# Optimization experiments

Measured on AMD Instinct MI355X. Metric: run time of the kernel, lower is better.

Reference implementation:

```python
import jax, jax.numpy as jnp
import numpy as np
import math

DIM = 1024
N_HEADS = 16
HEAD_DIM = DIM // N_HEADS  # 64
BATCH = 16
SEQ = 512


def _rope_tables(seq_len, head_dim, dtype=jnp.float32):
    inv_freq = 1.0 / (10000.0 ** (jnp.arange(0, head_dim, 2, dtype=jnp.float32) / head_dim))
    t = jnp.arange(seq_len, dtype=jnp.float32)
    freqs = jnp.outer(t, inv_freq)            # [S, head_dim/2]
    emb = jnp.concatenate([freqs, freqs], -1)  # [S, head_dim]
    return jnp.cos(emb).astype(dtype), jnp.sin(emb).astype(dtype)


def _rotate_half(x):
    x1, x2 = x[..., : x.shape[-1] // 2], x[..., x.shape[-1] // 2 :]
    return jnp.concatenate([-x2, x1], axis=-1)


def setup_inputs() -> dict:
    key = jax.random.key(0)
    ks = jax.random.split(key, 5)
    scale = 1.0 / math.sqrt(DIM)
    return {
        "x": jax.random.normal(ks[0], (BATCH, SEQ, DIM), dtype=jnp.float32),
        "Wq": jax.random.normal(ks[1], (DIM, DIM), dtype=jnp.float32) * scale,
        "Wk": jax.random.normal(ks[2], (DIM, DIM), dtype=jnp.float32) * scale,
        "Wv": jax.random.normal(ks[3], (DIM, DIM), dtype=jnp.float32) * scale,
        "Wo": jax.random.normal(ks[4], (DIM, DIM), dtype=jnp.float32) * scale,
    }


def reference(x, Wq, Wk, Wv, Wo):
    B, S, D = x.shape
    H, Hd = N_HEADS, HEAD_DIM
    # projections (nn.Linear: x @ W.T), then [B, H, S, Hd]
    q = (x @ Wq.T).reshape(B, S, H, Hd).transpose(0, 2, 1, 3)
    k = (x @ Wk.T).reshape(B, S, H, Hd).transpose(0, 2, 1, 3)
    v = (x @ Wv.T).reshape(B, S, H, Hd).transpose(0, 2, 1, 3)

    cos, sin = _rope_tables(S, Hd, x.dtype)  # [S, Hd], broadcasts over B, H
    q = q * cos + _rotate_half(q) * sin
    k = k * cos + _rotate_half(k) * sin

    scores = jnp.einsum("bhqd,bhkd->bhqk", q, k) / math.sqrt(Hd)
    causal = jnp.tril(jnp.ones((S, S), dtype=bool))
    scores = jnp.where(causal, scores, -jnp.inf)
    attn = jax.nn.softmax(scores, axis=-1)
    out = jnp.einsum("bhqk,bhkd->bhqd", attn, v)
    out = out.transpose(0, 2, 1, 3).reshape(B, S, D)
    return out @ Wo.T
```

## Files before the change

### kernel.cpp

```cpp
#include <hip/hip_runtime.h>

#define DIM 1024
#define NH 16
#define HD 64
#define BATCH 16
#define SEQ 512
#define MROWS (BATCH*SEQ)

using u16 = unsigned short;
using u32 = unsigned int;
typedef __attribute__((ext_vector_type(8))) u16 u16x8;
typedef __attribute__((ext_vector_type(4))) u16 u16x4;
typedef __attribute__((ext_vector_type(8))) __bf16 bf16x8;
typedef __attribute__((ext_vector_type(4))) float f32x4;
typedef __attribute__((ext_vector_type(4))) float float4v;

__device__ __forceinline__ float bf2f(u16 h) {
  unsigned u = ((unsigned)h) << 16;
  union { unsigned u; float f; } v; v.u = u; return v.f;
}
__device__ __forceinline__ u16 f2bf(float f) {
  union { float f; unsigned u; } v; v.f = f;
  unsigned u = v.u + 0x7fffu + ((v.u >> 16) & 1u);
  return (u16)(u >> 16);
}
__device__ __forceinline__ int swz(int r) { return (r & 7) ^ (r >> 3); }

__device__ __forceinline__ void gld_lds16(const u16* g, u16* l) {
  __builtin_amdgcn_global_load_lds(
      (const __attribute__((address_space(1))) void*)g,
      (__attribute__((address_space(3))) void*)l, 16, 0, 0);
}

__device__ __forceinline__ f32x4 mfma16(u16x8 a, u16x8 b, f32x4 c) {
  return __builtin_amdgcn_mfma_f32_16x16x32_bf16(
      __builtin_bit_cast(bf16x8, a), __builtin_bit_cast(bf16x8, b), c, 0, 0, 0);
}

__global__ void f32_to_bf16_kernel(const float* __restrict__ in, u16* __restrict__ out, int n) {
  int i = (blockIdx.x * blockDim.x + threadIdx.x) * 4;
  if (i >= n) return;
  float4v v = *(const float4v*)(in + i);
  u16x4 o;
  o.x = f2bf(v.x); o.y = f2bf(v.y); o.z = f2bf(v.z); o.w = f2bf(v.w);
  *(u16x4*)(out + i) = o;
}

__global__ void wconv_kernel(const float* __restrict__ Wq, const float* __restrict__ Wk,
                             const float* __restrict__ Wv, const float* __restrict__ Wo,
                             u16* __restrict__ out) {
  const float* in = (blockIdx.z == 0) ? Wq : (blockIdx.z == 1) ? Wk
                   : (blockIdx.z == 2) ? Wv : Wo;
  int i = (blockIdx.x * blockDim.x + threadIdx.x) * 4;
  float4v v = *(const float4v*)(in + i);
  u16x4 o;
  o.x = f2bf(v.x); o.y = f2bf(v.y); o.z = f2bf(v.z); o.w = f2bf(v.w);
  *(u16x4*)(out + (size_t)blockIdx.z * (DIM * DIM) + i) = o;
}

__global__ void rope_tables_kernel(float* __restrict__ ctab, float* __restrict__ stab) {
  int t = blockIdx.x * blockDim.x + threadIdx.x;
  int s = t >> 5, j = t & 31;
  float invf = powf(10000.f, -(float)j / 32.f);
  float a = (float)s * invf;
  ctab[t] = cosf(a);
  stab[t] = sinf(a);
}

__global__ void rope_kernel(u16* __restrict__ Q, u16* __restrict__ K,
                            const float* __restrict__ ctab, const float* __restrict__ stab) {
  int t = blockIdx.x * blockDim.x + threadIdx.x;
  u16* X = blockIdx.z ? K : Q;
  int j = t & 3;
  int h = (t >> 2) & 15;
  int m = t >> 6;
  int s = m & (SEQ - 1);
  u16* base = X + (size_t)m * DIM + h * HD + j * 8;
  u16x8 lo = *(u16x8*)base;
  u16x8 hi = *(u16x8*)(base + 32);
  const float* cp = ctab + s * 32 + j * 8;
  const float* sp = stab + s * 32 + j * 8;
  u16x8 lo2, hi2;
#pragma unroll
  for (int i = 0; i < 8; i++) {
    float c = cp[i], sn = sp[i];
    float xl = bf2f(lo[i]), xh = bf2f(hi[i]);
    lo2[i] = f2bf(xl * c - xh * sn);
    hi2[i] = f2bf(xh * c + xl * sn);
  }
  *(u16x8*)base = lo2;
  *(u16x8*)(base + 32) = hi2;
}

#define BM 128
#define BN 128

__global__ __launch_bounds__(256, 4) void gemm_qkv(const u16* __restrict__ A,
                                                   const u16* __restrict__ Bw,
                                                   u16* __restrict__ Cq, u16* __restrict__ Ck,
                                                   u16* __restrict__ Cv) {
  __shared__ alignas(16) u16 As[BM * 64];
  __shared__ alignas(16) u16 Bs[BN * 64];
  const int K = DIM, N = DIM;
  const int orig = blockIdx.x;
  const int id2 = (orig & 7) * 192 + (orig >> 3);
  const int m0 = (id2 / 24) * BM;
  const int n0g = (id2 % 24) * BN;
  u16* C = (n0g < 1024) ? Cq : (n0g < 2048) ? Ck : Cv;
  const int n0 = n0g & 1023;
  const int tid = threadIdx.x, lane = tid & 63;
  const int w = tid >> 6, wr = w >> 1, wc = w & 1;
  const int lr = lane & 15, kgrp = lane >> 4;

  f32x4 acc[4][4] = {};

  for (int kt = 0; kt < K; kt += 64) {
#pragma unroll
    for (int i = 0; i < 4; i++) {
      int c = tid + i * 256;
      int r_ = c >> 3, p = c & 7;
      gld_lds16(A + (size_t)(m0 + r_) * K + kt + ((p ^ (r_ & 7)) << 3), &As[c * 8]);
    }
#pragma unroll
    for (int i = 0; i < 4; i++) {
      int c = tid + i * 256;
      int r_ = c >> 3, p = c & 7;
      gld_lds16(Bw + (size_t)(n0g + r_) * K + kt + ((p ^ (r_ & 7)) << 3), &Bs[c * 8]);
    }
    __syncthreads();
#pragma unroll
    for (int half = 0; half < 2; half++) {
      u16x8 a[4], b[4];
      int g = half * 4 + kgrp;
#pragma unroll
      for (int i = 0; i < 4; i++) {
        int row = wr * 64 + i * 16 + lr;
        a[i] = *(const u16x8*)(&As[row * 64 + ((g ^ (row & 7)) << 3)]);
      }
#pragma unroll
      for (int j = 0; j < 4; j++) {
        int row = wc * 64 + j * 16 + lr;
        b[j] = *(const u16x8*)(&Bs[row * 64 + ((g ^ (row & 7)) << 3)]);
      }
#pragma unroll
      for (int i = 0; i < 4; i++)
#pragma unroll
        for (int j = 0; j < 4; j++)
          acc[i][j] = mfma16(a[i], b[j], acc[i][j]);
    }
    __syncthreads();
  }

#pragma unroll
  for (int i = 0; i < 4; i++) {
    int grow = m0 + wr * 64 + i * 16 + kgrp * 4;
#pragma unroll
    for (int j = 0; j < 4; j++) {
      int gcol = n0 + wc * 64 + j * 16 + lr;
#pragma unroll
      for (int r = 0; r < 4; r++)
        C[(size_t)(grow + r) * N + gcol] = f2bf(acc[i][j][r]);
    }
  }
}

__global__ __launch_bounds__(256, 4) void gemm_out(const u16* __restrict__ A,
                                                   const u16* __restrict__ B,
                                                   float* __restrict__ C) {
  __shared__ alignas(16) u16 As[BM * 64];
  __shared__ alignas(16) u16 Bs[BN * 64];
  const int K = DIM, N = DIM;
  const int orig = blockIdx.x;
  const int id2 = (orig & 7) * 64 + (orig >> 3);
  const int m0 = (id2 >> 3) * BM;
  const int n0 = (id2 & 7) * BN;
  const int tid = threadIdx.x, lane = tid & 63;
  const int w = tid >> 6, wr = w >> 1, wc = w & 1;
  const int lr = lane & 15, kgrp = lane >> 4;

  f32x4 acc[4][4] = {};

  for (int kt = 0; kt < K; kt += 64) {
#pragma unroll
    for (int i = 0; i < 4; i++) {
      int c = tid + i * 256;
      int r_ = c >> 3, p = c & 7;
      gld_lds16(A + (size_t)(m0 + r_) * K + kt + ((p ^ (r_ & 7)) << 3), &As[c * 8]);
    }
#pragma unroll
    for (int i = 0; i < 4; i++) {
      int c = tid + i * 256;
      int r_ = c >> 3, p = c & 7;
      gld_lds16(B + (size_t)(n0 + r_) * K + kt + ((p ^ (r_ & 7)) << 3), &Bs[c * 8]);
    }
    __syncthreads();
#pragma unroll
    for (int half = 0; half < 2; half++) {
      u16x8 a[4], b[4];
      int g = half * 4 + kgrp;
#pragma unroll
      for (int i = 0; i < 4; i++) {
        int row = wr * 64 + i * 16 + lr;
        a[i] = *(const u16x8*)(&As[row * 64 + ((g ^ (row & 7)) << 3)]);
      }
#pragma unroll
      for (int j = 0; j < 4; j++) {
        int row = wc * 64 + j * 16 + lr;
        b[j] = *(const u16x8*)(&Bs[row * 64 + ((g ^ (row & 7)) << 3)]);
      }
#pragma unroll
      for (int i = 0; i < 4; i++)
#pragma unroll
        for (int j = 0; j < 4; j++)
          acc[i][j] = mfma16(a[i], b[j], acc[i][j]);
    }
    __syncthreads();
  }

#pragma unroll
  for (int i = 0; i < 4; i++) {
    int grow = m0 + wr * 64 + i * 16 + kgrp * 4;
#pragma unroll
    for (int j = 0; j < 4; j++) {
      int gcol = n0 + wc * 64 + j * 16 + lr;
#pragma unroll
      for (int r = 0; r < 4; r++)
        C[(size_t)(grow + r) * N + gcol] = acc[i][j][r];
    }
  }
}

__global__ __launch_bounds__(256, 4) void attn_kernel(const u16* __restrict__ Q,
                                                      const u16* __restrict__ K,
                                                      const u16* __restrict__ V,
                                                      u16* __restrict__ O) {
  __shared__ alignas(16) u16 Ks[64 * 64];
  __shared__ alignas(16) u16 Vs[64 * 64];
  __shared__ alignas(16) u16 Vt[64 * 64];
  __shared__ alignas(16) u16 Ps[4][16 * 64];

  const int orig = blockIdx.x;
  const int id2 = (orig & 7) * 256 + (orig >> 3);
  const int qt = id2 & 7, bh = id2 >> 3;
  const int b = bh >> 4, h = bh & 15;
  const int tid = threadIdx.x, lane = tid & 63, w = tid >> 6;
  const int lr = lane & 15, kgrp = lane >> 4, koff = kgrp * 8;
  const int q0 = qt * 64;
  const int va = tid >> 3;
  const int vd = tid & 7;

  const u16* qptr = Q + ((size_t)(b * SEQ + q0 + w * 16 + lr)) * DIM + h * HD;
  u16x8 qf0 = *(const u16x8*)(qptr + koff);
  u16x8 qf1 = *(const u16x8*)(qptr + 32 + koff);

  f32x4 acc[4] = {};
  float mrow[4], lrow[4];
#pragma unroll
  for (int r = 0; r < 4; r++) { mrow[r] = -INFINITY; lrow[r] = 0.f; }

  const float scale = 0.125f;
  u32* Vt32 = (u32*)Vt;

  for (int kt = 0; kt <= qt; ++kt) {
    const u16* Kg = K + ((size_t)(b * SEQ + kt * 64)) * DIM + h * HD;
    const u16* Vg = V + ((size_t)(b * SEQ + kt * 64)) * DIM + h * HD;

#pragma unroll
    for (int i = 0; i < 2; i++) {
      int c = tid + i * 256;
      int r_ = c >> 3, p = c & 7;
      int ck = (p ^ swz(r_)) << 3;
      gld_lds16(Kg + (size_t)r_ * DIM + ck, &Ks[c * 8]);
      gld_lds16(Vg + (size_t)r_ * DIM + ck, &Vs[c * 8]);
    }
    __syncthreads();

    {
      int r0 = 2 * va, r1 = 2 * va + 1;
      u16x8 v0 = *(const u16x8*)(&Vs[r0 * 64 + ((vd ^ swz(r0)) << 3)]);
      u16x8 v1 = *(const u16x8*)(&Vs[r1 * 64 + ((vd ^ swz(r1)) << 3)]);
#pragma unroll
      for (int i = 0; i < 8; i++) {
        int d = vd * 8 + i;
        u32 val = (u32)v0[i] | ((u32)v1[i] << 16);
        Vt32[d * 32 + (((va >> 2) ^ swz(d)) << 2) + (va & 3)] = val;
      }
    }

    f32x4 sacc[4] = {};
#pragma unroll
    for (int j = 0; j < 4; j++) {
      int row = j * 16 + lr;
      int p0 = kgrp ^ swz(row);
      u16x8 kf0 = *(const u16x8*)(&Ks[row * 64 + p0 * 8]);
      u16x8 kf1 = *(const u16x8*)(&Ks[row * 64 + (p0 ^ 4) * 8]);
      sacc[j] = mfma16(qf0, kf0, sacc[j]);
      sacc[j] = mfma16(qf1, kf1, sacc[j]);
    }

    if (kt == qt) {
#pragma unroll
      for (int j = 0; j < 4; j++)
#pragma unroll
        for (int r = 0; r < 4; r++) {
          float s = sacc[j][r] * scale;
          if (j * 16 + lr > w * 16 + kgrp * 4 + r) s = -1e30f;
          sacc[j][r] = s;
        }
    } else {
#pragma unroll
      for (int j = 0; j < 4; j++)
#pragma unroll
        for (int r = 0; r < 4; r++) sacc[j][r] *= scale;
    }

#pragma unroll
    for (int r = 0; r < 4; r++) {
      float mx = fmaxf(fmaxf(sacc[0][r], sacc[1][r]), fmaxf(sacc[2][r], sacc[3][r]));
#pragma unroll
      for (int off = 1; off < 16; off <<= 1) mx = fmaxf(mx, __shfl_xor(mx, off, 64));
      float mnew = fmaxf(mrow[r], mx);
      float f = __expf(mrow[r] - mnew);
      mrow[r] = mnew;
      lrow[r] *= f;
#pragma unroll
      for (int j = 0; j < 4; j++) acc[j][r] *= f;
      float s0 = 0.f;
#pragma unroll
      for (int j = 0; j < 4; j++) { float p = __expf(sacc[j][r] - mnew); sacc[j][r] = p; s0 += p; }
#pragma unroll
      for (int off = 1; off < 16; off <<= 1) s0 += __shfl_xor(s0, off, 64);
      lrow[r] += s0;
    }

#pragma unroll
    for (int j = 0; j < 4; j++) {
      int gk = 2 * j + (lr >> 3);
#pragma unroll
      for (int r = 0; r < 4; r++) {
        int q = kgrp * 4 + r;
        Ps[w][q * 64 + ((gk ^ swz(q)) << 3) + (lr & 7)] = f2bf(sacc[j][r]);
      }
    }

    __syncthreads();

#pragma unroll
    for (int ks = 0; ks < 2; ++ks) {
      int g = ks * 4 + kgrp;
      u16x8 pa = *(const u16x8*)(&Ps[w][lr * 64 + ((g ^ swz(lr)) << 3)]);
#pragma unroll
      for (int j = 0; j < 4; j++) {
        int d = j * 16 + lr;
        u16x8 vb = *(const u16x8*)(&Vt[d * 64 + ((g ^ swz(d)) << 3)]);
        acc[j] = mfma16(pa, vb, acc[j]);
      }
    }
  }

  const size_t rowbase = (size_t)(b * SEQ + q0 + w * 16);
#pragma unroll
  for (int r = 0; r < 4; r++) {
    float inv = 1.f / lrow[r];
    u16* op = O + (rowbase + kgrp * 4 + r) * DIM + h * HD;
#pragma unroll
    for (int j = 0; j < 4; j++) op[j * 16 + lr] = f2bf(acc[j][r] * inv);
  }
}

extern "C" void kernel_launch(void* const* d_in, const int* in_sizes, int n_in,
                              void* d_out, int out_size, void* d_ws, size_t ws_size,
                              hipStream_t stream) {
  const float* x  = (const float*)d_in[0];
  const float* Wq = (const float*)d_in[1];
  const float* Wk = (const float*)d_in[2];
  const float* Wv = (const float*)d_in[3];
  const float* Wo = (const float*)d_in[4];
  float* out = (float*)d_out;

  char* ws = (char*)d_ws;
  u16* xb    = (u16*)(ws);
  u16* qb    = (u16*)(ws + 16777216);
  u16* kb    = (u16*)(ws + 33554432);
  u16* vb    = (u16*)(ws + 50331648);
  u16* attnb = (u16*)(ws + 67108864);
  u16* wqb   = (u16*)(ws + 83886080);
  u16* wkb   = (u16*)(ws + 85983232);
  u16* wvb   = (u16*)(ws + 88080384);
  u16* wob   = (u16*)(ws + 90177536);
  float* ctab = (float*)(ws + 92274688);
  float* stab = (float*)(ws + 92340224);

  const int nx = MROWS * DIM;
  const int nw = DIM * DIM;

  f32_to_bf16_kernel<<<nx / 4 / 256, 256, 0, stream>>>(x, xb, nx);
  wconv_kernel<<<dim3(nw / 4 / 256, 1, 4), 256, 0, stream>>>(Wq, Wk, Wv, Wo, wqb);
  rope_tables_kernel<<<SEQ * 32 / 256, 256, 0, stream>>>(ctab, stab);

  gemm_qkv<<<1536, 256, 0, stream>>>(xb, wqb, qb, kb, vb);

  rope_kernel<<<dim3(MROWS * NH * 4 / 256, 1, 2), 256, 0, stream>>>(qb, kb, ctab, stab);

  attn_kernel<<<2048, 256, 0, stream>>>(qb, kb, vb, attnb);

  gemm_out<<<512, 256, 0, stream>>>(attnb, wob, out);
}
```

Baseline: 249.2 us.

## Fuse RoPE into QKV GEMM epilogue and process two query tiles per attention block

The separate RoPE pass over Q and K is removed. Rotation is now applied in fp32 on the QKV GEMM accumulators before bf16 rounding, which saves a full read-modify-write of Q and K. The attention kernel now handles 128 query rows per block as two 64-row chunks, so each K/V tile load and V transpose is shared by both chunks, and the grid is halved. It also adds s_setprio around the MFMA sections. The trade-off is more registers and LDS per block and fewer blocks, which may reduce occupancy and make causal load balance coarser.

```diff
diff --git a/kernel.cpp b/kernel.cpp
--- a/kernel.cpp
+++ b/kernel.cpp
@@ -67,38 +67,15 @@
   stab[t] = sinf(a);
 }
 
-__global__ void rope_kernel(u16* __restrict__ Q, u16* __restrict__ K,
-                            const float* __restrict__ ctab, const float* __restrict__ stab) {
-  int t = blockIdx.x * blockDim.x + threadIdx.x;
-  u16* X = blockIdx.z ? K : Q;
-  int j = t & 3;
-  int h = (t >> 2) & 15;
-  int m = t >> 6;
-  int s = m & (SEQ - 1);
-  u16* base = X + (size_t)m * DIM + h * HD + j * 8;
-  u16x8 lo = *(u16x8*)base;
-  u16x8 hi = *(u16x8*)(base + 32);
-  const float* cp = ctab + s * 32 + j * 8;
-  const float* sp = stab + s * 32 + j * 8;
-  u16x8 lo2, hi2;
-#pragma unroll
-  for (int i = 0; i < 8; i++) {
-    float c = cp[i], sn = sp[i];
-    float xl = bf2f(lo[i]), xh = bf2f(hi[i]);
-    lo2[i] = f2bf(xl * c - xh * sn);
-    hi2[i] = f2bf(xh * c + xl * sn);
-  }
-  *(u16x8*)base = lo2;
-  *(u16x8*)(base + 32) = hi2;
-}
-
 #define BM 128
 #define BN 128
 
 __global__ __launch_bounds__(256, 4) void gemm_qkv(const u16* __restrict__ A,
                                                    const u16* __restrict__ Bw,
                                                    u16* __restrict__ Cq, u16* __restrict__ Ck,
-                                                   u16* __restrict__ Cv) {
+                                                   u16* __restrict__ Cv,
+                                                   const float* __restrict__ ctab,
+                                                   const float* __restrict__ stab) {
   __shared__ alignas(16) u16 As[BM * 64];
   __shared__ alignas(16) u16 Bs[BN * 64];
   const int K = DIM, N = DIM;
@@ -149,6 +126,25 @@
           acc[i][j] = mfma16(a[i], b[j], acc[i][j]);
     }
     __syncthreads();
+  }
+
+  if (n0g < 2048) {
+#pragma unroll
+    for (int i = 0; i < 4; i++) {
+      int grow = m0 + wr * 64 + i * 16 + kgrp * 4;
+#pragma unroll
+      for (int r = 0; r < 4; r++) {
+        int s = (grow + r) & (SEQ - 1);
+#pragma unroll
+        for (int j = 0; j < 2; j++) {
+          float c = ctab[s * 32 + j * 16 + lr];
+          float sn = stab[s * 32 + j * 16 + lr];
+          float a0 = acc[i][j][r], a1 = acc[i][j + 2][r];
+          acc[i][j][r] = a0 * c - a1 * sn;
+          acc[i][j + 2][r] = a1 * c + a0 * sn;
+        }
+      }
+    }
   }
 
 #pragma unroll
@@ -237,31 +233,38 @@
   __shared__ alignas(16) u16 Ks[64 * 64];
   __shared__ alignas(16) u16 Vs[64 * 64];
   __shared__ alignas(16) u16 Vt[64 * 64];
-  __shared__ alignas(16) u16 Ps[4][16 * 64];
+  __shared__ alignas(16) u16 Ps[4][2][16 * 64];
 
   const int orig = blockIdx.x;
-  const int id2 = (orig & 7) * 256 + (orig >> 3);
-  const int qt = id2 & 7, bh = id2 >> 3;
+  const int id2 = (orig & 7) * 128 + (orig >> 3);
+  const int qt2 = id2 & 3, bh = id2 >> 2;
   const int b = bh >> 4, h = bh & 15;
   const int tid = threadIdx.x, lane = tid & 63, w = tid >> 6;
   const int lr = lane & 15, kgrp = lane >> 4, koff = kgrp * 8;
-  const int q0 = qt * 64;
+  const int q0 = qt2 * 128;
   const int va = tid >> 3;
   const int vd = tid & 7;
 
-  const u16* qptr = Q + ((size_t)(b * SEQ + q0 + w * 16 + lr)) * DIM + h * HD;
-  u16x8 qf0 = *(const u16x8*)(qptr + koff);
-  u16x8 qf1 = *(const u16x8*)(qptr + 32 + koff);
-
-  f32x4 acc[4] = {};
-  float mrow[4], lrow[4];
-#pragma unroll
-  for (int r = 0; r < 4; r++) { mrow[r] = -INFINITY; lrow[r] = 0.f; }
+  u16x8 qf0[2], qf1[2];
+#pragma unroll
+  for (int cc = 0; cc < 2; cc++) {
+    const u16* qptr = Q + ((size_t)(b * SEQ + q0 + cc * 64 + w * 16 + lr)) * DIM + h * HD;
+    qf0[cc] = *(const u16x8*)(qptr + koff);
+    qf1[cc] = *(const u16x8*)(qptr + 32 + koff);
+  }
+
+  f32x4 acc[2][4] = {};
+  float mrow[2][4], lrow[2][4];
+#pragma unroll
+  for (int cc = 0; cc < 2; cc++)
+#pragma unroll
+    for (int r = 0; r < 4; r++) { mrow[cc][r] = -INFINITY; lrow[cc][r] = 0.f; }
 
   const float scale = 0.125f;
   u32* Vt32 = (u32*)Vt;
-
-  for (int kt = 0; kt <= qt; ++kt) {
+  const int ktmax = 2 * qt2 + 1;
+
+  for (int kt = 0; kt <= ktmax; ++kt) {
     const u16* Kg = K + ((size_t)(b * SEQ + kt * 64)) * DIM + h * HD;
     const u16* Vg = V + ((size_t)(b * SEQ + kt * 64)) * DIM + h * HD;
 
@@ -287,84 +290,100 @@
       }
     }
 
-    f32x4 sacc[4] = {};
-#pragma unroll
-    for (int j = 0; j < 4; j++) {
-      int row = j * 16 + lr;
-      int p0 = kgrp ^ swz(row);
-      u16x8 kf0 = *(const u16x8*)(&Ks[row * 64 + p0 * 8]);
-      u16x8 kf1 = *(const u16x8*)(&Ks[row * 64 + (p0 ^ 4) * 8]);
-      sacc[j] = mfma16(qf0, kf0, sacc[j]);
-      sacc[j] = mfma16(qf1, kf1, sacc[j]);
-    }
-
-    if (kt == qt) {
-#pragma unroll
-      for (int j = 0; j < 4; j++)
+#pragma unroll
+    for (int cc = 0; cc < 2; cc++) {
+      if (cc == 0 && kt > 2 * qt2) continue;
+
+      f32x4 sacc[4] = {};
+      __builtin_amdgcn_s_setprio(1);
+#pragma unroll
+      for (int j = 0; j < 4; j++) {
+        int row = j * 16 + lr;
+        int p0 = kgrp ^ swz(row);
+        u16x8 kf0 = *(const u16x8*)(&Ks[row * 64 + p0 * 8]);
+        u16x8 kf1 = *(const u16x8*)(&Ks[row * 64 + (p0 ^ 4) * 8]);
+        sacc[j] = mfma16(qf0[cc], kf0, sacc[j]);
+        sacc[j] = mfma16(qf1[cc], kf1, sacc[j]);
+      }
+      __builtin_amdgcn_s_setprio(0);
+
+      if (kt == 2 * qt2 + cc) {
+#pragma unroll
+        for (int j = 0; j < 4; j++)
+#pragma unroll
+          for (int r = 0; r < 4; r++) {
+            float s = sacc[j][r] * scale;
+            if (j * 16 + lr > w * 16 + kgrp * 4 + r) s = -1e30f;
+            sacc[j][r] = s;
+          }
+      } else {
+#pragma unroll
+        for (int j = 0; j < 4; j++)
+#pragma unroll
+          for (int r = 0; r < 4; r++) sacc[j][r] *= scale;
+      }
+
+#pragma unroll
+      for (int r = 0; r < 4; r++) {
+        float mx = fmaxf(fmaxf(sacc[0][r], sacc[1][r]), fmaxf(sacc[2][r], sacc[3][r]));
+#pragma unroll
+        for (int off = 1; off < 16; off <<= 1) mx = fmaxf(mx, __shfl_xor(mx, off, 64));
+        float mnew = fmaxf(mrow[cc][r], mx);
+        float f = __expf(mrow[cc][r] - mnew);
+        mrow[cc][r] = mnew;
+        lrow[cc][r] *= f;
+#pragma unroll
+        for (int j = 0; j < 4; j++) acc[cc][j][r] *= f;
+        float s0 = 0.f;
+#pragma unroll
+        for (int j = 0; j < 4; j++) { float p = __expf(sacc[j][r] - mnew); sacc[j][r] = p; s0 += p; }
+#pragma unroll
+        for (int off = 1; off < 16; off <<= 1) s0 += __shfl_xor(s0, off, 64);
+        lrow[cc][r] += s0;
+      }
+
+#pragma unroll
+      for (int j = 0; j < 4; j++) {
+        int gk = 2 * j + (lr >> 3);
 #pragma unroll
         for (int r = 0; r < 4; r++) {
-          float s = sacc[j][r] * scale;
-          if (j * 16 + lr > w * 16 + kgrp * 4 + r) s = -1e30f;
-          sacc[j][r] = s;
+          int q = kgrp * 4 + r;
+          Ps[w][cc][q * 64 + ((gk ^ swz(q)) << 3) + (lr & 7)] = f2bf(sacc[j][r]);
         }
-    } else {
-#pragma unroll
-      for (int j = 0; j < 4; j++)
-#pragma unroll
-        for (int r = 0; r < 4; r++) sacc[j][r] *= scale;
-    }
-
+      }
+    }
+
+    __syncthreads();
+
+#pragma unroll
+    for (int cc = 0; cc < 2; cc++) {
+      if (cc == 0 && kt > 2 * qt2) continue;
+      __builtin_amdgcn_s_setprio(1);
+#pragma unroll
+      for (int ks = 0; ks < 2; ++ks) {
+        int g = ks * 4 + kgrp;
+        u16x8 pa = *(const u16x8*)(&Ps[w][cc][lr * 64 + ((g ^ swz(lr)) << 3)]);
+#pragma unroll
+        for (int j = 0; j < 4; j++) {
+          int d = j * 16 + lr;
+          u16x8 vb = *(const u16x8*)(&Vt[d * 64 + ((g ^ swz(d)) << 3)]);
+          acc[cc][j] = mfma16(pa, vb, acc[cc][j]);
+        }
+      }
+      __builtin_amdgcn_s_setprio(0);
+    }
+  }
+
+#pragma unroll
+  for (int cc = 0; cc < 2; cc++) {
+    const size_t rowbase = (size_t)(b * SEQ + q0 + cc * 64 + w * 16);
 #pragma unroll
     for (int r = 0; r < 4; r++) {
-      float mx = fmaxf(fmaxf(sacc[0][r], sacc[1][r]), fmaxf(sacc[2][r], sacc[3][r]));
-#pragma unroll
-      for (int off = 1; off < 16; off <<= 1) mx = fmaxf(mx, __shfl_xor(mx, off, 64));
-      float mnew = fmaxf(mrow[r], mx);
-      float f = __expf(mrow[r] - mnew);
-      mrow[r] = mnew;
-      lrow[r] *= f;
-#pragma unroll
-      for (int j = 0; j < 4; j++) acc[j][r] *= f;
-      float s0 = 0.f;
-#pragma unroll
-      for (int j = 0; j < 4; j++) { float p = __expf(sacc[j][r] - mnew); sacc[j][r] = p; s0 += p; }
-#pragma unroll
-      for (int off = 1; off < 16; off <<= 1) s0 += __shfl_xor(s0, off, 64);
-      lrow[r] += s0;
-    }
-
-#pragma unroll
-    for (int j = 0; j < 4; j++) {
-      int gk = 2 * j + (lr >> 3);
-#pragma unroll
-      for (int r = 0; r < 4; r++) {
-        int q = kgrp * 4 + r;
-        Ps[w][q * 64 + ((gk ^ swz(q)) << 3) + (lr & 7)] = f2bf(sacc[j][r]);
-      }
-    }
-
-    __syncthreads();
-
-#pragma unroll
-    for (int ks = 0; ks < 2; ++ks) {
-      int g = ks * 4 + kgrp;
-      u16x8 pa = *(const u16x8*)(&Ps[w][lr * 64 + ((g ^ swz(lr)) << 3)]);
-#pragma unroll
-      for (int j = 0; j < 4; j++) {
-        int d = j * 16 + lr;
-        u16x8 vb = *(const u16x8*)(&Vt[d * 64 + ((g ^ swz(d)) << 3)]);
-        acc[j] = mfma16(pa, vb, acc[j]);
-      }
-    }
-  }
-
-  const size_t rowbase = (size_t)(b * SEQ + q0 + w * 16);
-#pragma unroll
-  for (int r = 0; r < 4; r++) {
-    float inv = 1.f / lrow[r];
-    u16* op = O + (rowbase + kgrp * 4 + r) * DIM + h * HD;
-#pragma unroll
-    for (int j = 0; j < 4; j++) op[j * 16 + lr] = f2bf(acc[j][r] * inv);
+      float inv = 1.f / lrow[cc][r];
+      u16* op = O + (rowbase + kgrp * 4 + r) * DIM + h * HD;
+#pragma unroll
+      for (int j = 0; j < 4; j++) op[j * 16 + lr] = f2bf(acc[cc][j][r] * inv);
+    }
   }
 }
 
@@ -385,8 +404,6 @@
   u16* vb    = (u16*)(ws + 50331648);
   u16* attnb = (u16*)(ws + 67108864);
   u16* wqb   = (u16*)(ws + 83886080);
-  u16* wkb   = (u16*)(ws + 85983232);
-  u16* wvb   = (u16*)(ws + 88080384);
   u16* wob   = (u16*)(ws + 90177536);
   float* ctab = (float*)(ws + 92274688);
   float* stab = (float*)(ws + 92340224);
@@ -398,11 +415,9 @@
   wconv_kernel<<<dim3(nw / 4 / 256, 1, 4), 256, 0, stream>>>(Wq, Wk, Wv, Wo, wqb);
   rope_tables_kernel<<<SEQ * 32 / 256, 256, 0, stream>>>(ctab, stab);
 
-  gemm_qkv<<<1536, 256, 0, stream>>>(xb, wqb, qb, kb, vb);
-
-  rope_kernel<<<dim3(MROWS * NH * 4 / 256, 1, 2), 256, 0, stream>>>(qb, kb, ctab, stab);
-
-  attn_kernel<<<2048, 256, 0, stream>>>(qb, kb, vb, attnb);
+  gemm_qkv<<<1536, 256, 0, stream>>>(xb, wqb, qb, kb, vb, ctab, stab);
+
+  attn_kernel<<<1024, 256, 0, stream>>>(qb, kb, vb, attnb);
 
   gemm_out<<<512, 256, 0, stream>>>(attnb, wob, out);
 }
```

Measured after the change: 299.4 us. +20.1%, slower.
